# Optimization experiments

Hardware: AMD Instinct MI355X
Metric: run time of the kernel (lower is better)

Reference implementation:

```python
import jax, jax.numpy as jnp
import numpy as np


def setup_inputs() -> dict:
    key = jax.random.key(0)
    k1, k2, k3, k4 = jax.random.split(key, 4)
    B, S, H, D = 4, 2048, 1024, 1024
    X = jax.random.normal(k1, (B, S, H), dtype=jnp.float32)
    # nn.Linear weight stored as [out, in]; we store as [in, out] for x @ W
    scale = 1.0 / np.sqrt(H)
    Wq = jax.random.normal(k2, (H, D), dtype=jnp.float32) * scale
    Wk = jax.random.normal(k3, (H, D), dtype=jnp.float32) * scale
    Wv = jax.random.normal(k4, (H, D), dtype=jnp.float32) * scale
    return {"X": X, "Wq": Wq, "Wk": Wk, "Wv": Wv}


def reference(X, Wq, Wk, Wv):
    B, S, H = X.shape
    q = X @ Wq  # [B, S, D]
    k = X @ Wk
    v = X @ Wv
    D = k.shape[-1]
    scores = jnp.einsum('bqd,bkd->bqk', q, k) / jnp.sqrt(jnp.float32(D))
    causal = jnp.tril(jnp.ones((S, S), dtype=bool))  # block_size mask sliced to S
    scores = jnp.where(causal, scores, -jnp.inf)
    weights = jax.nn.softmax(scores, axis=-1)  # dropout p=0.0 -> identity
    return jnp.einsum('bqk,bkd->bqd', weights, v)
```

## Files before the change

### kernel.cpp

```cpp
#include <hip/hip_runtime.h>

#define AS1 __attribute__((address_space(1)))
#define AS3 __attribute__((address_space(3)))

typedef __attribute__((ext_vector_type(8))) short short8;
typedef __attribute__((ext_vector_type(4))) float floatx4;

__device__ __forceinline__ short f2bf(float f) {
  union { float f; unsigned u; } v; v.f = f;
  return (short)((v.u + 0x7fffu + ((v.u >> 16) & 1u)) >> 16);
}
__device__ __forceinline__ float bf2f(short s) {
  union { unsigned u; float f; } v; v.u = ((unsigned)(unsigned short)s) << 16;
  return v.f;
}

__device__ __forceinline__ void gload_lds16(const void* g, void* l) {
  __builtin_amdgcn_global_load_lds((const AS1 unsigned*)g, (AS3 unsigned*)l, 16, 0, 0);
}

__device__ __forceinline__ void stage128x64(const short* __restrict__ G, long rowBase, long ld,
                                            int kBase, short* lds, int lane, int wave) {
  const int chunk = (lane & 7) ^ ((lane >> 3) & 7);
  const short* gb = G + rowBase * ld + (long)kBase + (long)(lane >> 3) * ld + chunk * 8;
#pragma unroll
  for (int j = 0; j < 4; ++j) {
    int c = wave * 4 + j;
    gload_lds16(gb + (long)c * 8 * ld, lds + c * 512);
  }
}

__device__ __forceinline__ short8 lds_rd(const short* l, int row, int kk, int lane) {
  const int r = row + (lane & 15);
  const int c = (kk + ((lane >> 4) << 3)) ^ ((lane & 7) << 3);
  return *(const short8*)(l + r * 64 + c);
}

#define MEMFENCE() asm volatile("" ::: "memory")
#define SBAR() do { MEMFENCE(); __builtin_amdgcn_s_barrier(); MEMFENCE(); } while (0)
#define SCHEDB() __builtin_amdgcn_sched_barrier(0)

__device__ const unsigned char PAIR72[72] = {
  0x00,
  0x10,
  0x20,0x21,
  0x30,0x31,
  0x40,0x41,0x42,
  0x50,0x51,0x52,
  0x60,0x61,0x62,0x63,
  0x70,0x71,0x72,0x73,
  0x80,0x81,0x82,0x83,0x84,
  0x90,0x91,0x92,0x93,0x94,
  0xA0,0xA1,0xA2,0xA3,0xA4,0xA5,
  0xB0,0xB1,0xB2,0xB3,0xB4,0xB5,
  0xC0,0xC1,0xC2,0xC3,0xC4,0xC5,0xC6,
  0xD0,0xD1,0xD2,0xD3,0xD4,0xD5,0xD6,
  0xE0,0xE1,0xE2,0xE3,0xE4,0xE5,0xE6,0xE7,
  0xF0,0xF1,0xF2,0xF3,0xF4,0xF5,0xF6,0xF7
};

__global__ void prep_inputs(const float* __restrict__ X, const float* __restrict__ Wq,
                            const float* __restrict__ Wk, const float* __restrict__ Wv,
                            short* __restrict__ Xb, short* __restrict__ Wt,
                            float* __restrict__ l) {
  __shared__ float t[32][33];
  if (blockIdx.x < 8192) {
    long i = ((long)blockIdx.x * 256 + threadIdx.x) * 4;
    float4 v = *(const float4*)(X + i);
    short4 o;
    o.x = f2bf(v.x); o.y = f2bf(v.y); o.z = f2bf(v.z); o.w = f2bf(v.w);
    *(short4*)(Xb + i) = o;
  } else if (blockIdx.x < 11264) {
    int idx = blockIdx.x - 8192;
    int z = idx >> 10, rem = idx & 1023;
    int bx = rem >> 5, by = rem & 31;
    const float* W = z == 0 ? Wq : (z == 1 ? Wk : Wv);
    short* O = Wt + (long)z * 1024 * 1024;
    int tx = threadIdx.x & 31, ty = threadIdx.x >> 5;
    int x = bx * 32 + tx;
    int y0 = by * 32;
    for (int j = ty; j < 32; j += 8)
      t[j][tx] = W[(long)(y0 + j) * 1024 + x];
    __syncthreads();
    int x2 = by * 32 + tx;
    int y2 = bx * 32;
    for (int j = ty; j < 32; j += 8)
      O[(long)(y2 + j) * 1024 + x2] = f2bf(t[tx][j]);
  } else {
    l[(blockIdx.x - 11264) * 256 + threadIdx.x] = 0.0f;
  }
}

#define LOFF(b, m, h) ((((b) * 2 + (m)) * 2 + (h)) * 8192)

__device__ __forceinline__ void stage_half(const short* __restrict__ g, short* l, int wv) {
  gload_lds16(g, l + wv * 512);
  gload_lds16(g + 65536, l + 4096 + wv * 512);
}

__global__ __launch_bounds__(512, 2) void gemm_qkv(const short* __restrict__ Xb,
                                                   const short* __restrict__ Wt,
                                                   short* __restrict__ Q, short* __restrict__ K2,
                                                   short* __restrict__ Vt) {
  __shared__ __align__(16) short lds[65536];
  const int tid = threadIdx.x;
  const int lane = tid & 63, wv = tid >> 6;
  const int wm = wv >> 2, wn = wv & 3;

  const int bid = blockIdx.x;
  const int xcd = bid & 7, w = bid >> 3;
  const int mt = xcd * 4 + (w / 12);
  const int ng = w % 12;
  const int z = ng >> 2;
  const long mBase = (long)mt * 256;
  const long nBase = (long)(ng & 3) * 256;
  const short* Bm = Wt + (long)z * 1048576;

  const int r0 = tid >> 3;
  const int cc = ((tid & 7) ^ (r0 & 7)) << 3;
  const short* gA = Xb + (mBase + r0) * 1024 + cc;
  const short* gB = Bm + (nBase + r0) * 1024 + cc;

  floatx4 acc[8][4];
  const floatx4 zero = {0.f, 0.f, 0.f, 0.f};
#pragma unroll
  for (int i = 0; i < 8; ++i)
#pragma unroll
    for (int j = 0; j < 4; ++j) acc[i][j] = zero;

  short8 a0[4][2], a1[4][2], bq[2][2];

  stage_half(gA, lds + LOFF(0, 0, 0), wv);
  stage_half(gA + 131072, lds + LOFF(0, 0, 1), wv);
  stage_half(gB, lds + LOFF(0, 1, 0), wv);
  stage_half(gB + 131072, lds + LOFF(0, 1, 1), wv);
  stage_half(gA + 64, lds + LOFF(1, 0, 0), wv);
  stage_half(gA + 64 + 131072, lds + LOFF(1, 0, 1), wv);
  stage_half(gB + 64, lds + LOFF(1, 1, 0), wv);
  asm volatile("s_waitcnt vmcnt(6)" ::: "memory");
  SBAR();
  {
    const short* Ab0 = lds + LOFF(0, 0, wm);
#pragma unroll
    for (int f = 0; f < 4; ++f) a0[f][0] = lds_rd(Ab0, f * 16, 0, lane);
#pragma unroll
    for (int f = 0; f < 4; ++f) a0[f][1] = lds_rd(Ab0, f * 16, 32, lane);
  }

#pragma unroll 2
  for (int t = 0; t < 16; ++t) {
    const int buf = t & 1;
    const short* Ab  = lds + LOFF(buf, 0, wm);
    const short* Bb  = lds + LOFF(buf, 1, (wn >> 1));
    const short* AbN = lds + LOFF(buf ^ 1, 0, wm);
    const int brow = (wn & 1) * 64;

    bq[0][0] = lds_rd(Bb, brow, 0, lane);
    bq[1][0] = lds_rd(Bb, brow + 16, 0, lane);
    bq[0][1] = lds_rd(Bb, brow, 32, lane);
    bq[1][1] = lds_rd(Bb, brow + 16, 32, lane);
#pragma unroll
    for (int f = 0; f < 4; ++f) a1[f][0] = lds_rd(Ab, 64 + f * 16, 0, lane);
#pragma unroll
    for (int f = 0; f < 4; ++f) a1[f][1] = lds_rd(Ab, 64 + f * 16, 32, lane);
    if (t < 15) stage_half(gB + (t + 1) * 64 + 131072, lds + LOFF(buf ^ 1, 1, 1), wv);
    asm volatile("s_waitcnt lgkmcnt(8)" ::: "memory");
    SCHEDB();
    __builtin_amdgcn_s_setprio(1);
#pragma unroll
    for (int f = 0; f < 4; ++f)
#pragma unroll
      for (int n = 0; n < 2; ++n)
        acc[f][n] = __builtin_amdgcn_mfma_f32_16x16x32_bf16(a0[f][0], bq[n][0], acc[f][n], 0, 0, 0);
#pragma unroll
    for (int f = 0; f < 4; ++f)
#pragma unroll
      for (int n = 0; n < 2; ++n)
        acc[f][n] = __builtin_amdgcn_mfma_f32_16x16x32_bf16(a0[f][1], bq[n][1], acc[f][n], 0, 0, 0);
    __builtin_amdgcn_s_setprio(0);

    asm volatile("s_waitcnt lgkmcnt(0)" ::: "memory");
    SCHEDB();
    __builtin_amdgcn_s_setprio(1);
#pragma unroll
    for (int f = 0; f < 4; ++f)
#pragma unroll
      for (int n = 0; n < 2; ++n)
        acc[4 + f][n] = __builtin_amdgcn_mfma_f32_16x16x32_bf16(a1[f][0], bq[n][0], acc[4 + f][n], 0, 0, 0);
#pragma unroll
    for (int f = 0; f < 4; ++f)
#pragma unroll
      for (int n = 0; n < 2; ++n)
        acc[4 + f][n] = __builtin_amdgcn_mfma_f32_16x16x32_bf16(a1[f][1], bq[n][1], acc[4 + f][n], 0, 0, 0);
    __builtin_amdgcn_s_setprio(0);
    SBAR();

    bq[0][0] = lds_rd(Bb, brow + 32, 0, lane);
    bq[1][0] = lds_rd(Bb, brow + 48, 0, lane);
    bq[0][1] = lds_rd(Bb, brow + 32, 32, lane);
    bq[1][1] = lds_rd(Bb, brow + 48, 32, lane);
    if (t < 14) stage_half(gA + (t + 2) * 64, lds + LOFF(buf, 0, 0), wv);
    asm volatile("s_waitcnt lgkmcnt(0)" ::: "memory");
    SCHEDB();
    __builtin_amdgcn_s_setprio(1);
#pragma unroll
    for (int f = 0; f < 4; ++f)
#pragma unroll
      for (int n = 0; n < 2; ++n)
        acc[f][2 + n] = __builtin_amdgcn_mfma_f32_16x16x32_bf16(a0[f][0], bq[n][0], acc[f][2 + n], 0, 0, 0);
#pragma unroll
    for (int f = 0; f < 4; ++f)
#pragma unroll
      for (int n = 0; n < 2; ++n)
        acc[f][2 + n] = __builtin_amdgcn_mfma_f32_16x16x32_bf16(a0[f][1], bq[n][1], acc[f][2 + n], 0, 0, 0);
    __builtin_amdgcn_s_setprio(0);
    if (t < 14) { asm volatile("s_waitcnt vmcnt(2)" ::: "memory"); }
    else        { asm volatile("s_waitcnt vmcnt(0)" ::: "memory"); }
    SBAR();

    if (t < 15) {
#pragma unroll
      for (int f = 0; f < 4; ++f) a0[f][0] = lds_rd(AbN, f * 16, 0, lane);
#pragma unroll
      for (int f = 0; f < 4; ++f) a0[f][1] = lds_rd(AbN, f * 16, 32, lane);
    }
    if (t < 14) {
      stage_half(gA + (t + 2) * 64 + 131072, lds + LOFF(buf, 0, 1), wv);
      stage_half(gB + (t + 2) * 64, lds + LOFF(buf, 1, 0), wv);
    }
    SCHEDB();
    __builtin_amdgcn_s_setprio(1);
#pragma unroll
    for (int f = 0; f < 4; ++f)
#pragma unroll
      for (int n = 0; n < 2; ++n)
        acc[4 + f][2 + n] = __builtin_amdgcn_mfma_f32_16x16x32_bf16(a1[f][0], bq[n][0], acc[4 + f][2 + n], 0, 0, 0);
#pragma unroll
    for (int f = 0; f < 4; ++f)
#pragma unroll
      for (int n = 0; n < 2; ++n)
        acc[4 + f][2 + n] = __builtin_amdgcn_mfma_f32_16x16x32_bf16(a1[f][1], bq[n][1], acc[4 + f][2 + n], 0, 0, 0);
    __builtin_amdgcn_s_setprio(0);
  }

  if (z < 2) {
    short* outp = (z == 0) ? Q : K2;
#pragma unroll
    for (int f = 0; f < 8; ++f)
#pragma unroll
      for (int n = 0; n < 4; ++n) {
        const int col = (int)nBase + wn * 64 + n * 16 + (lane & 15);
#pragma unroll
        for (int rr = 0; rr < 4; ++rr) {
          const long m = mBase + wm * 128 + f * 16 + ((lane >> 4) << 2) + rr;
          outp[m * 1024 + col] = f2bf(acc[f][n][rr]);
        }
      }
  } else {
    const long bz = mBase >> 11;
    const int sB = (int)(mBase & 2047);
#pragma unroll
    for (int f = 0; f < 8; ++f) {
      const int s0 = sB + wm * 128 + f * 16 + ((lane >> 4) << 2);
#pragma unroll
      for (int n = 0; n < 4; ++n) {
        const int col = (int)nBase + wn * 64 + n * 16 + (lane & 15);
        short4 o;
        o.x = f2bf(acc[f][n][0]); o.y = f2bf(acc[f][n][1]);
        o.z = f2bf(acc[f][n][2]); o.w = f2bf(acc[f][n][3]);
        *(short4*)(Vt + ((bz * 1024 + col) * 2048 + s0)) = o;
      }
    }
  }
}

__global__ __launch_bounds__(256, 2) void scores_exp(const short* __restrict__ Q,
                                                     const short* __restrict__ Kk,
                                                     short* __restrict__ E, float* __restrict__ l) {
  __shared__ __align__(16) short lds[24576];
  short* lQ = lds;
  short* lK0 = lds + 8192;
  short* lK1 = lds + 16384;
  const int lane = threadIdx.x & 63, wave = threadIdx.x >> 6;
  const int wm = wave >> 1, wn = wave & 1;
  const int b = blockIdx.y;

  const int cls = blockIdx.x & 7, idx = blockIdx.x >> 3;
  const int code = PAIR72[cls * 9 + idx];
  const int qt = code >> 4, ktp = code & 15;
  const int kt0 = ktp * 2, kt1 = kt0 + 1;
  const bool two = (kt1 <= qt);

  const long rowQ = (long)b * 2048 + (long)qt * 128;
  const long rowK0 = (long)b * 2048 + (long)kt0 * 128;
  const long rowK1 = rowK0 + 128;

  floatx4 acc0[4][4], acc1[4][4];
  const floatx4 zero = {0.f, 0.f, 0.f, 0.f};
#pragma unroll
  for (int i = 0; i < 4; ++i)
#pragma unroll
    for (int j = 0; j < 4; ++j) { acc0[i][j] = zero; acc1[i][j] = zero; }

  for (int it = 0; it < 16; ++it) {
    stage128x64(Q, rowQ, 1024, it * 64, lQ, lane, wave);
    stage128x64(Kk, rowK0, 1024, it * 64, lK0, lane, wave);
    if (two) stage128x64(Kk, rowK1, 1024, it * 64, lK1, lane, wave);
    __syncthreads();
    short8 a[4][2], bb[4][2];
#pragma unroll
    for (int i = 0; i < 4; ++i) {
      a[i][0] = lds_rd(lQ, wm * 64 + i * 16, 0, lane);
      a[i][1] = lds_rd(lQ, wm * 64 + i * 16, 32, lane);
    }
#pragma unroll
    for (int i = 0; i < 4; ++i) {
      bb[i][0] = lds_rd(lK0, wn * 64 + i * 16, 0, lane);
      bb[i][1] = lds_rd(lK0, wn * 64 + i * 16, 32, lane);
    }
#pragma unroll
    for (int ks = 0; ks < 2; ++ks)
#pragma unroll
      for (int i = 0; i < 4; ++i)
#pragma unroll
        for (int j = 0; j < 4; ++j)
          acc0[i][j] = __builtin_amdgcn_mfma_f32_16x16x32_bf16(a[i][ks], bb[j][ks], acc0[i][j], 0, 0, 0);
    if (two) {
#pragma unroll
      for (int i = 0; i < 4; ++i) {
        bb[i][0] = lds_rd(lK1, wn * 64 + i * 16, 0, lane);
        bb[i][1] = lds_rd(lK1, wn * 64 + i * 16, 32, lane);
      }
#pragma unroll
      for (int ks = 0; ks < 2; ++ks)
#pragma unroll
        for (int i = 0; i < 4; ++i)
#pragma unroll
          for (int j = 0; j < 4; ++j)
            acc1[i][j] = __builtin_amdgcn_mfma_f32_16x16x32_bf16(a[i][ks], bb[j][ks], acc1[i][j], 0, 0, 0);
    }
    __syncthreads();
  }

  short* lbuf = lds;
  float* lrow = l + (long)b * 2048;
  short* Eb = E + (long)b * 4194304;
#pragma unroll 1
  for (int tsel = 0; tsel < 2; ++tsel) {
    if (tsel == 1 && !two) break;
    const int kt = tsel == 0 ? kt0 : kt1;
    floatx4 (&acc)[4][4] = tsel == 0 ? acc0 : acc1;
    if (tsel == 1) __syncthreads();
#pragma unroll
    for (int i = 0; i < 4; ++i) {
#pragma unroll
      for (int rr = 0; rr < 4; ++rr) {
        int ri = wm * 64 + i * 16 + (lane >> 4) * 4 + rr;
        int qrow = qt * 128 + ri;
        float psum = 0.f;
#pragma unroll
        for (int j = 0; j < 4; ++j) {
          int ci = wn * 64 + j * 16 + (lane & 15);
          int col = kt * 128 + ci;
          float sc = acc[i][j][rr] * 0.03125f;
          float e = (col <= qrow) ? __expf(sc) : 0.0f;
          short eb = f2bf(e);
          lbuf[ri * 128 + ((((ci >> 3) ^ (ri & 15)) << 3) | (ci & 7))] = eb;
          psum += bf2f(eb);
        }
        for (int m = 1; m < 16; m <<= 1) psum += __shfl_xor(psum, m, 64);
        if ((lane & 15) == 0) atomicAdd(&lrow[qrow], psum);
      }
    }
    __syncthreads();
    const long ebase = (long)(qt * 128) * 2048 + kt * 128;
#pragma unroll
    for (int pp = 0; pp < 8; ++pp) {
      int g = pp * 256 + threadIdx.x;
      int row = g >> 4, c = g & 15;
      short8 v = *(const short8*)(lbuf + row * 128 + ((c ^ (row & 15)) << 3));
      *(short8*)(Eb + ebase + (long)row * 2048 + c * 8) = v;
    }
  }
}

__global__ __launch_bounds__(256, 2) void pv_gemm(const short* __restrict__ E,
                                                  const short* __restrict__ Vt,
                                                  const float* __restrict__ l,
                                                  float* __restrict__ part,
                                                  float* __restrict__ out) {
  __shared__ __align__(16) short lds[24576];
  short* lE = lds;
  short* lV0 = lds + 8192;
  short* lV1 = lds + 16384;
  const int lane = threadIdx.x & 63, wave = threadIdx.x >> 6;
  const int wm = wave >> 1, wn = wave & 1;
  const int x = blockIdx.x;
  const int xcd = x & 7, w = x >> 3;
  const int dt0 = xcd >> 1, dt1 = dt0 + 4;
  const int within = (xcd & 1) * 12 + w;
  const int r = within & 7, wsel = within >> 3;
  const int b = blockIdx.y;

  int qt, it0, it1, mode;
  if (wsel == 2) {
    qt = r; it0 = 0; it1 = (qt + 1) * 2; mode = 0;
  } else {
    qt = 15 - r;
    const int T = (qt + 1) * 2, c0 = T >> 1;
    if (wsel == 0) { it0 = 0;  it1 = c0; mode = 1; }
    else           { it0 = c0; it1 = T;  mode = 2; }
  }

  const short* Eb = E + (long)b * 2048 * 2048;
  const short* Vb = Vt + (long)b * 1024 * 2048;
  const float* lrow = l + (long)b * 2048;
  const long rowE = (long)qt * 128;
  const long rowV0 = (long)dt0 * 128, rowV1 = (long)dt1 * 128;

  floatx4 acc0[4][4], acc1[4][4];
  const floatx4 zero = {0.f, 0.f, 0.f, 0.f};
#pragma unroll
  for (int i = 0; i < 4; ++i)
#pragma unroll
    for (int j = 0; j < 4; ++j) { acc0[i][j] = zero; acc1[i][j] = zero; }

  for (int it = it0; it < it1; ++it) {
    stage128x64(Eb, rowE, 2048, it * 64, lE, lane, wave);
    stage128x64(Vb, rowV0, 2048, it * 64, lV0, lane, wave);
    stage128x64(Vb, rowV1, 2048, it * 64, lV1, lane, wave);
    __syncthreads();
    short8 a[4][2], bb[4][2];
#pragma unroll
    for (int i = 0; i < 4; ++i) {
      a[i][0] = lds_rd(lE, wm * 64 + i * 16, 0, lane);
      a[i][1] = lds_rd(lE, wm * 64 + i * 16, 32, lane);
    }
#pragma unroll
    for (int i = 0; i < 4; ++i) {
      bb[i][0] = lds_rd(lV0, wn * 64 + i * 16, 0, lane);
      bb[i][1] = lds_rd(lV0, wn * 64 + i * 16, 32, lane);
    }
#pragma unroll
    for (int ks = 0; ks < 2; ++ks)
#pragma unroll
      for (int i = 0; i < 4; ++i)
#pragma unroll
        for (int j = 0; j < 4; ++j)
          acc0[i][j] = __builtin_amdgcn_mfma_f32_16x16x32_bf16(a[i][ks], bb[j][ks], acc0[i][j], 0, 0, 0);
#pragma unroll
    for (int i = 0; i < 4; ++i) {
      bb[i][0] = lds_rd(lV1, wn * 64 + i * 16, 0, lane);
      bb[i][1] = lds_rd(lV1, wn * 64 + i * 16, 32, lane);
    }
#pragma unroll
    for (int ks = 0; ks < 2; ++ks)
#pragma unroll
      for (int i = 0; i < 4; ++i)
#pragma unroll
        for (int j = 0; j < 4; ++j)
          acc1[i][j] = __builtin_amdgcn_mfma_f32_16x16x32_bf16(a[i][ks], bb[j][ks], acc1[i][j], 0, 0, 0);
    __syncthreads();
  }

  if (mode == 2) {
    float* P0 = part + ((((long)b * 8 + (qt - 8)) * 8 + dt0) << 14);
    float* P1 = part + ((((long)b * 8 + (qt - 8)) * 8 + dt1) << 14);
#pragma unroll
    for (int i = 0; i < 4; ++i)
#pragma unroll
      for (int rr = 0; rr < 4; ++rr) {
        int ri = wm * 64 + i * 16 + (lane >> 4) * 4 + rr;
#pragma unroll
        for (int j = 0; j < 4; ++j) {
          int ci = wn * 64 + j * 16 + (lane & 15);
          P0[ri * 128 + ci] = acc0[i][j][rr];
          P1[ri * 128 + ci] = acc1[i][j][rr];
        }
      }
  } else {
#pragma unroll
    for (int i = 0; i < 4; ++i)
#pragma unroll
      for (int rr = 0; rr < 4; ++rr) {
        int qrow = qt * 128 + wm * 64 + i * 16 + (lane >> 4) * 4 + rr;
        float scale = (mode == 0) ? 1.0f / lrow[qrow] : 1.0f;
#pragma unroll
        for (int j = 0; j < 4; ++j) {
          int ci = wn * 64 + j * 16 + (lane & 15);
          out[((long)b * 2048 + qrow) * 1024 + dt0 * 128 + ci] = acc0[i][j][rr] * scale;
          out[((long)b * 2048 + qrow) * 1024 + dt1 * 128 + ci] = acc1[i][j][rr] * scale;
        }
      }
  }
}

__global__ void pv_reduce(float* __restrict__ out, const float* __restrict__ part,
                          const float* __restrict__ l) {
  const int idx = blockIdx.x;
  const int b = idx >> 10;
  const int row = 1024 + (idx & 1023);
  const int t = threadIdx.x;
  const int dt = t >> 5, dl = (t << 2) & 127;
  const float inv = 1.0f / l[((long)b << 11) + row];
  const long pbase = ((((long)b * 8 + ((row >> 7) - 8)) * 8 + dt) << 14) + ((row & 127) << 7) + dl;
  const long obase = (((long)b * 2048 + row) << 10) + (t << 2);
  float4 o = *(const float4*)(out + obase);
  float4 p = *(const float4*)(part + pbase);
  o.x = (o.x + p.x) * inv; o.y = (o.y + p.y) * inv;
  o.z = (o.z + p.z) * inv; o.w = (o.w + p.w) * inv;
  *(float4*)(out + obase) = o;
}

extern "C" void kernel_launch(void* const* d_in, const int* in_sizes, int n_in,
                              void* d_out, int out_size, void* d_ws, size_t ws_size,
                              hipStream_t stream) {
  const float* X  = (const float*)d_in[0];
  const float* Wq = (const float*)d_in[1];
  const float* Wk = (const float*)d_in[2];
  const float* Wv = (const float*)d_in[3];

  char* ws = (char*)d_ws;
  short* Xb = (short*)(ws);
  short* Wt = (short*)(ws + 16777216L);
  short* Q  = (short*)(ws + 23068672L);
  short* K2 = (short*)(ws + 39845888L);
  short* Vt = (short*)(ws + 56623104L);
  short* E  = (short*)(ws + 73400320L);
  float* l  = (float*)(ws + 106954752L);
  float* part = (float*)(ws);

  prep_inputs<<<11296, 256, 0, stream>>>(X, Wq, Wk, Wv, Xb, Wt, l);
  gemm_qkv<<<384, 512, 0, stream>>>(Xb, Wt, Q, K2, Vt);
  scores_exp<<<dim3(72, 4), 256, 0, stream>>>(Q, K2, E, l);
  pv_gemm<<<dim3(96, 4), 256, 0, stream>>>(E, Vt, l, part, (float*)d_out);
  pv_reduce<<<4096, 256, 0, stream>>>((float*)d_out, part, l);
}
```

Before: 230.9 us.

## Rewrite scores kernel with 256x256 triangular tiles and pipelined LDS staging

The causal QK^T plus exp kernel moves from 128x128 tile pairs at 256 threads to 256x256 triangular tiles at 512 threads. The K loop now uses double-buffered asynchronous global-to-LDS staging, explicit waitcnt and sched barriers, and setprio around MFMA bursts, so loads overlap with compute. The goal is more reuse per loaded byte and better hiding of load latency. In exchange the grid drops to 144 blocks, which may leave CUs idle. The larger diagonal tiles also spend more work on masked entries, and the 128KB of LDS limits each CU to one block.

```diff
diff --git a/kernel.cpp b/kernel.cpp
--- a/kernel.cpp
+++ b/kernel.cpp
@@ -40,23 +40,15 @@
 #define SBAR() do { MEMFENCE(); __builtin_amdgcn_s_barrier(); MEMFENCE(); } while (0)
 #define SCHEDB() __builtin_amdgcn_sched_barrier(0)
 
-__device__ const unsigned char PAIR72[72] = {
+__device__ const unsigned char TRI36[36] = {
   0x00,
-  0x10,
-  0x20,0x21,
-  0x30,0x31,
-  0x40,0x41,0x42,
-  0x50,0x51,0x52,
-  0x60,0x61,0x62,0x63,
-  0x70,0x71,0x72,0x73,
-  0x80,0x81,0x82,0x83,0x84,
-  0x90,0x91,0x92,0x93,0x94,
-  0xA0,0xA1,0xA2,0xA3,0xA4,0xA5,
-  0xB0,0xB1,0xB2,0xB3,0xB4,0xB5,
-  0xC0,0xC1,0xC2,0xC3,0xC4,0xC5,0xC6,
-  0xD0,0xD1,0xD2,0xD3,0xD4,0xD5,0xD6,
-  0xE0,0xE1,0xE2,0xE3,0xE4,0xE5,0xE6,0xE7,
-  0xF0,0xF1,0xF2,0xF3,0xF4,0xF5,0xF6,0xF7
+  0x10,0x11,
+  0x20,0x21,0x22,
+  0x30,0x31,0x32,0x33,
+  0x40,0x41,0x42,0x43,0x44,
+  0x50,0x51,0x52,0x53,0x54,0x55,
+  0x60,0x61,0x62,0x63,0x64,0x65,0x66,
+  0x70,0x71,0x72,0x73,0x74,0x75,0x76,0x77
 };
 
 __global__ void prep_inputs(const float* __restrict__ X, const float* __restrict__ Wq,
@@ -274,112 +266,180 @@
   }
 }
 
-__global__ __launch_bounds__(256, 2) void scores_exp(const short* __restrict__ Q,
+__global__ __launch_bounds__(512, 2) void scores_exp(const short* __restrict__ Q,
                                                      const short* __restrict__ Kk,
                                                      short* __restrict__ E, float* __restrict__ l) {
-  __shared__ __align__(16) short lds[24576];
-  short* lQ = lds;
-  short* lK0 = lds + 8192;
-  short* lK1 = lds + 16384;
-  const int lane = threadIdx.x & 63, wave = threadIdx.x >> 6;
-  const int wm = wave >> 1, wn = wave & 1;
+  __shared__ __align__(16) short lds[65536];
+  const int tid = threadIdx.x;
+  const int lane = tid & 63, wv = tid >> 6;
+  const int wm = wv >> 2, wn = wv & 3;
+
+  const int code = TRI36[blockIdx.x];
+  const int qtt = code >> 4, ktt = code & 15;
   const int b = blockIdx.y;
 
-  const int cls = blockIdx.x & 7, idx = blockIdx.x >> 3;
-  const int code = PAIR72[cls * 9 + idx];
-  const int qt = code >> 4, ktp = code & 15;
-  const int kt0 = ktp * 2, kt1 = kt0 + 1;
-  const bool two = (kt1 <= qt);
-
-  const long rowQ = (long)b * 2048 + (long)qt * 128;
-  const long rowK0 = (long)b * 2048 + (long)kt0 * 128;
-  const long rowK1 = rowK0 + 128;
-
-  floatx4 acc0[4][4], acc1[4][4];
+  const int r0 = tid >> 3;
+  const int cc = ((tid & 7) ^ (r0 & 7)) << 3;
+  const short* gA = Q  + ((long)b * 2048 + (long)qtt * 256 + r0) * 1024 + cc;
+  const short* gB = Kk + ((long)b * 2048 + (long)ktt * 256 + r0) * 1024 + cc;
+
+  floatx4 acc[8][4];
   const floatx4 zero = {0.f, 0.f, 0.f, 0.f};
 #pragma unroll
-  for (int i = 0; i < 4; ++i)
-#pragma unroll
-    for (int j = 0; j < 4; ++j) { acc0[i][j] = zero; acc1[i][j] = zero; }
-
-  for (int it = 0; it < 16; ++it) {
-    stage128x64(Q, rowQ, 1024, it * 64, lQ, lane, wave);
-    stage128x64(Kk, rowK0, 1024, it * 64, lK0, lane, wave);
-    if (two) stage128x64(Kk, rowK1, 1024, it * 64, lK1, lane, wave);
-    __syncthreads();
-    short8 a[4][2], bb[4][2];
-#pragma unroll
-    for (int i = 0; i < 4; ++i) {
-      a[i][0] = lds_rd(lQ, wm * 64 + i * 16, 0, lane);
-      a[i][1] = lds_rd(lQ, wm * 64 + i * 16, 32, lane);
-    }
-#pragma unroll
-    for (int i = 0; i < 4; ++i) {
-      bb[i][0] = lds_rd(lK0, wn * 64 + i * 16, 0, lane);
-      bb[i][1] = lds_rd(lK0, wn * 64 + i * 16, 32, lane);
-    }
-#pragma unroll
-    for (int ks = 0; ks < 2; ++ks)
-#pragma unroll
-      for (int i = 0; i < 4; ++i)
-#pragma unroll
-        for (int j = 0; j < 4; ++j)
-          acc0[i][j] = __builtin_amdgcn_mfma_f32_16x16x32_bf16(a[i][ks], bb[j][ks], acc0[i][j], 0, 0, 0);
-    if (two) {
-#pragma unroll
-      for (int i = 0; i < 4; ++i) {
-        bb[i][0] = lds_rd(lK1, wn * 64 + i * 16, 0, lane);
-        bb[i][1] = lds_rd(lK1, wn * 64 + i * 16, 32, lane);
-      }
-#pragma unroll
-      for (int ks = 0; ks < 2; ++ks)
-#pragma unroll
-        for (int i = 0; i < 4; ++i)
-#pragma unroll
-          for (int j = 0; j < 4; ++j)
-            acc1[i][j] = __builtin_amdgcn_mfma_f32_16x16x32_bf16(a[i][ks], bb[j][ks], acc1[i][j], 0, 0, 0);
-    }
-    __syncthreads();
-  }
-
-  short* lbuf = lds;
+  for (int i = 0; i < 8; ++i)
+#pragma unroll
+    for (int j = 0; j < 4; ++j) acc[i][j] = zero;
+
+  short8 a0[4][2], a1[4][2], bq[2][2];
+
+  stage_half(gA, lds + LOFF(0, 0, 0), wv);
+  stage_half(gA + 131072, lds + LOFF(0, 0, 1), wv);
+  stage_half(gB, lds + LOFF(0, 1, 0), wv);
+  stage_half(gB + 131072, lds + LOFF(0, 1, 1), wv);
+  stage_half(gA + 64, lds + LOFF(1, 0, 0), wv);
+  stage_half(gA + 64 + 131072, lds + LOFF(1, 0, 1), wv);
+  stage_half(gB + 64, lds + LOFF(1, 1, 0), wv);
+  asm volatile("s_waitcnt vmcnt(6)" ::: "memory");
+  SBAR();
+  {
+    const short* Ab0 = lds + LOFF(0, 0, wm);
+#pragma unroll
+    for (int f = 0; f < 4; ++f) a0[f][0] = lds_rd(Ab0, f * 16, 0, lane);
+#pragma unroll
+    for (int f = 0; f < 4; ++f) a0[f][1] = lds_rd(Ab0, f * 16, 32, lane);
+  }
+
+#pragma unroll 2
+  for (int t = 0; t < 16; ++t) {
+    const int buf = t & 1;
+    const short* Ab  = lds + LOFF(buf, 0, wm);
+    const short* Bb  = lds + LOFF(buf, 1, (wn >> 1));
+    const short* AbN = lds + LOFF(buf ^ 1, 0, wm);
+    const int brow = (wn & 1) * 64;
+
+    bq[0][0] = lds_rd(Bb, brow, 0, lane);
+    bq[1][0] = lds_rd(Bb, brow + 16, 0, lane);
+    bq[0][1] = lds_rd(Bb, brow, 32, lane);
+    bq[1][1] = lds_rd(Bb, brow + 16, 32, lane);
+#pragma unroll
+    for (int f = 0; f < 4; ++f) a1[f][0] = lds_rd(Ab, 64 + f * 16, 0, lane);
+#pragma unroll
+    for (int f = 0; f < 4; ++f) a1[f][1] = lds_rd(Ab, 64 + f * 16, 32, lane);
+    if (t < 15) stage_half(gB + (t + 1) * 64 + 131072, lds + LOFF(buf ^ 1, 1, 1), wv);
+    asm volatile("s_waitcnt lgkmcnt(8)" ::: "memory");
+    SCHEDB();
+    __builtin_amdgcn_s_setprio(1);
+#pragma unroll
+    for (int f = 0; f < 4; ++f)
+#pragma unroll
+      for (int n = 0; n < 2; ++n)
+        acc[f][n] = __builtin_amdgcn_mfma_f32_16x16x32_bf16(a0[f][0], bq[n][0], acc[f][n], 0, 0, 0);
+#pragma unroll
+    for (int f = 0; f < 4; ++f)
+#pragma unroll
+      for (int n = 0; n < 2; ++n)
+        acc[f][n] = __builtin_amdgcn_mfma_f32_16x16x32_bf16(a0[f][1], bq[n][1], acc[f][n], 0, 0, 0);
+    __builtin_amdgcn_s_setprio(0);
+
+    asm volatile("s_waitcnt lgkmcnt(0)" ::: "memory");
+    SCHEDB();
+    __builtin_amdgcn_s_setprio(1);
+#pragma unroll
+    for (int f = 0; f < 4; ++f)
+#pragma unroll
+      for (int n = 0; n < 2; ++n)
+        acc[4 + f][n] = __builtin_amdgcn_mfma_f32_16x16x32_bf16(a1[f][0], bq[n][0], acc[4 + f][n], 0, 0, 0);
+#pragma unroll
+    for (int f = 0; f < 4; ++f)
+#pragma unroll
+      for (int n = 0; n < 2; ++n)
+        acc[4 + f][n] = __builtin_amdgcn_mfma_f32_16x16x32_bf16(a1[f][1], bq[n][1], acc[4 + f][n], 0, 0, 0);
+    __builtin_amdgcn_s_setprio(0);
+    SBAR();
+
+    bq[0][0] = lds_rd(Bb, brow + 32, 0, lane);
+    bq[1][0] = lds_rd(Bb, brow + 48, 0, lane);
+    bq[0][1] = lds_rd(Bb, brow + 32, 32, lane);
+    bq[1][1] = lds_rd(Bb, brow + 48, 32, lane);
+    if (t < 14) stage_half(gA + (t + 2) * 64, lds + LOFF(buf, 0, 0), wv);
+    asm volatile("s_waitcnt lgkmcnt(0)" ::: "memory");
+    SCHEDB();
+    __builtin_amdgcn_s_setprio(1);
+#pragma unroll
+    for (int f = 0; f < 4; ++f)
+#pragma unroll
+      for (int n = 0; n < 2; ++n)
+        acc[f][2 + n] = __builtin_amdgcn_mfma_f32_16x16x32_bf16(a0[f][0], bq[n][0], acc[f][2 + n], 0, 0, 0);
+#pragma unroll
+    for (int f = 0; f < 4; ++f)
+#pragma unroll
+      for (int n = 0; n < 2; ++n)
+        acc[f][2 + n] = __builtin_amdgcn_mfma_f32_16x16x32_bf16(a0[f][1], bq[n][1], acc[f][2 + n], 0, 0, 0);
+    __builtin_amdgcn_s_setprio(0);
+    if (t < 14) { asm volatile("s_waitcnt vmcnt(2)" ::: "memory"); }
+    else        { asm volatile("s_waitcnt vmcnt(0)" ::: "memory"); }
+    SBAR();
+
+    if (t < 15) {
+#pragma unroll
+      for (int f = 0; f < 4; ++f) a0[f][0] = lds_rd(AbN, f * 16, 0, lane);
+#pragma unroll
+      for (int f = 0; f < 4; ++f) a0[f][1] = lds_rd(AbN, f * 16, 32, lane);
+    }
+    if (t < 14) {
+      stage_half(gA + (t + 2) * 64 + 131072, lds + LOFF(buf, 0, 1), wv);
+      stage_half(gB + (t + 2) * 64, lds + LOFF(buf, 1, 0), wv);
+    }
+    SCHEDB();
+    __builtin_amdgcn_s_setprio(1);
+#pragma unroll
+    for (int f = 0; f < 4; ++f)
+#pragma unroll
+      for (int n = 0; n < 2; ++n)
+        acc[4 + f][2 + n] = __builtin_amdgcn_mfma_f32_16x16x32_bf16(a1[f][0], bq[n][0], acc[4 + f][2 + n], 0, 0, 0);
+#pragma unroll
+    for (int f = 0; f < 4; ++f)
+#pragma unroll
+      for (int n = 0; n < 2; ++n)
+        acc[4 + f][2 + n] = __builtin_amdgcn_mfma_f32_16x16x32_bf16(a1[f][1], bq[n][1], acc[4 + f][2 + n], 0, 0, 0);
+    __builtin_amdgcn_s_setprio(0);
+  }
+
   float* lrow = l + (long)b * 2048;
   short* Eb = E + (long)b * 4194304;
 #pragma unroll 1
-  for (int tsel = 0; tsel < 2; ++tsel) {
-    if (tsel == 1 && !two) break;
-    const int kt = tsel == 0 ? kt0 : kt1;
-    floatx4 (&acc)[4][4] = tsel == 0 ? acc0 : acc1;
-    if (tsel == 1) __syncthreads();
-#pragma unroll
-    for (int i = 0; i < 4; ++i) {
-#pragma unroll
-      for (int rr = 0; rr < 4; ++rr) {
-        int ri = wm * 64 + i * 16 + (lane >> 4) * 4 + rr;
-        int qrow = qt * 128 + ri;
-        float psum = 0.f;
-#pragma unroll
-        for (int j = 0; j < 4; ++j) {
-          int ci = wn * 64 + j * 16 + (lane & 15);
-          int col = kt * 128 + ci;
-          float sc = acc[i][j][rr] * 0.03125f;
-          float e = (col <= qrow) ? __expf(sc) : 0.0f;
-          short eb = f2bf(e);
-          lbuf[ri * 128 + ((((ci >> 3) ^ (ri & 15)) << 3) | (ci & 7))] = eb;
-          psum += bf2f(eb);
+  for (int kh = 0; kh < 2; ++kh) {
+    SBAR();
+    if ((wn >> 1) == kh) {
+#pragma unroll
+      for (int f = 0; f < 8; ++f) {
+#pragma unroll
+        for (int rr = 0; rr < 4; ++rr) {
+          const int ri = wm * 128 + f * 16 + ((lane >> 4) << 2) + rr;
+          const int qrow = qtt * 256 + ri;
+          float psum = 0.f;
+#pragma unroll
+          for (int n = 0; n < 4; ++n) {
+            const int cil = (wn & 1) * 64 + n * 16 + (lane & 15);
+            const int col = ktt * 256 + kh * 128 + cil;
+            float sc = acc[f][n][rr] * 0.03125f;
+            float e = (col <= qrow) ? __expf(sc) : 0.0f;
+            short eb = f2bf(e);
+            lds[ri * 128 + ((((cil >> 3) ^ (ri & 15)) << 3) | (cil & 7))] = eb;
+            psum += bf2f(eb);
+          }
+          for (int m = 1; m < 16; m <<= 1) psum += __shfl_xor(psum, m, 64);
+          if ((lane & 15) == 0) atomicAdd(&lrow[qrow], psum);
         }
-        for (int m = 1; m < 16; m <<= 1) psum += __shfl_xor(psum, m, 64);
-        if ((lane & 15) == 0) atomicAdd(&lrow[qrow], psum);
       }
     }
-    __syncthreads();
-    const long ebase = (long)(qt * 128) * 2048 + kt * 128;
-#pragma unroll
-    for (int pp = 0; pp < 8; ++pp) {
-      int g = pp * 256 + threadIdx.x;
+    SBAR();
+#pragma unroll
+    for (int p = 0; p < 8; ++p) {
+      int g = p * 512 + tid;
       int row = g >> 4, c = g & 15;
-      short8 v = *(const short8*)(lbuf + row * 128 + ((c ^ (row & 15)) << 3));
-      *(short8*)(Eb + ebase + (long)row * 2048 + c * 8) = v;
+      short8 v = *(const short8*)(lds + row * 128 + ((c ^ (row & 15)) << 3));
+      *(short8*)(Eb + (long)(qtt * 256 + row) * 2048 + ktt * 256 + kh * 128 + c * 8) = v;
     }
   }
 }
@@ -532,7 +592,7 @@
 
   prep_inputs<<<11296, 256, 0, stream>>>(X, Wq, Wk, Wv, Xb, Wt, l);
   gemm_qkv<<<384, 512, 0, stream>>>(Xb, Wt, Q, K2, Vt);
-  scores_exp<<<dim3(72, 4), 256, 0, stream>>>(Q, K2, E, l);
+  scores_exp<<<dim3(36, 4), 512, 0, stream>>>(Q, K2, E, l);
   pv_gemm<<<dim3(96, 4), 256, 0, stream>>>(E, Vt, l, part, (float*)d_out);
   pv_reduce<<<4096, 256, 0, stream>>>((float*)d_out, part, l);
 }
```

New measurement: 297.6 us. +28.9%, slower.
